# Kernel tuning notes

Measured on AMD Instinct MI355X. Metric: run time of the kernel, lower is better.

Reference implementation:

```python
import jax, jax.numpy as jnp
import numpy as np

RNN = 400
K_WIN = 10      # num_window_mixtures
N_MIX = 20      # num_mixtures
ALPHA = 80      # alphabet_size
IN2 = RNN + ALPHA + 3  # lstm2/lstm3 input size = 483
MDN_OUT = 1 + 6 * N_MIX  # 121


def setup_inputs() -> dict:
    key = jax.random.key(0)
    ks = jax.random.split(key, 20)
    std = 0.075
    B, T, U = 256, 800, 100
    inp = {
        "trajectory": jax.random.normal(ks[0], (B, T, 3), jnp.float32),
        "char_sequence": jax.random.uniform(ks[1], (B, U, ALPHA), jnp.float32),
        # LSTM1 (input 3)
        "w_ih1": jax.random.normal(ks[2], (4 * RNN, 3), jnp.float32) * std,
        "w_hh1": jax.random.normal(ks[3], (4 * RNN, RNN), jnp.float32) * std,
        "b1": jax.random.normal(ks[4], (4 * RNN,), jnp.float32) * std,
        # LSTM2 (input 483)
        "w_ih2": jax.random.normal(ks[5], (4 * RNN, IN2), jnp.float32) * std,
        "w_hh2": jax.random.normal(ks[6], (4 * RNN, RNN), jnp.float32) * std,
        "b2": jax.random.normal(ks[7], (4 * RNN,), jnp.float32) * std,
        # LSTM3 (input 483)
        "w_ih3": jax.random.normal(ks[8], (4 * RNN, IN2), jnp.float32) * std,
        "w_hh3": jax.random.normal(ks[9], (4 * RNN, RNN), jnp.float32) * std,
        "b3": jax.random.normal(ks[10], (4 * RNN,), jnp.float32) * std,
        # window linear (Graves attention), bias init mean -3.0 std 0.25
        "w_win": jax.random.normal(ks[11], (3 * K_WIN, RNN), jnp.float32) * std,
        "b_win": jax.random.normal(ks[12], (3 * K_WIN,), jnp.float32) * 0.25 - 3.0,
        # MDN head
        "w_mdn": jax.random.normal(ks[13], (MDN_OUT, RNN), jnp.float32) * std,
        "b_mdn": jax.random.normal(ks[14], (MDN_OUT,), jnp.float32) * std,
    }
    return inp


def _lstm_cell(x, h, c, w_ih, w_hh, b):
    # torch.nn.LSTMCell gate order: i, f, g, o
    gates = x @ w_ih.T + h @ w_hh.T + b
    i, f, g, o = jnp.split(gates, 4, axis=-1)
    c_new = jax.nn.sigmoid(f) * c + jax.nn.sigmoid(i) * jnp.tanh(g)
    h_new = jax.nn.sigmoid(o) * jnp.tanh(c_new)
    return h_new, c_new


def reference(trajectory, char_sequence,
              w_ih1, w_hh1, b1, w_ih2, w_hh2, b2, w_ih3, w_hh3, b3,
              w_win, b_win, w_mdn, b_mdn):
    B, T, _ = trajectory.shape
    U = char_sequence.shape[1]
    u = jnp.arange(U, dtype=trajectory.dtype)  # [U]

    def step(carry, x_t):
        h1, c1, h2, c2, h3, c3, kappa = carry
        h1, c1 = _lstm_cell(x_t, h1, c1, w_ih1, w_hh1, b1)
        # Gaussian-window attention
        wp = jnp.exp(h1 @ w_win.T + b_win).reshape(B, 3, K_WIN)
        alpha, beta, dkappa = wp[:, 0], wp[:, 1], wp[:, 2]
        kappa = kappa + dkappa
        # phi: [B, U] = sum_k alpha_k * exp(-beta_k * (kappa_k - u)^2)
        diff = kappa[:, :, None] - u[None, None, :]          # [B, K, U]
        phi = jnp.sum(alpha[:, :, None] * jnp.exp(-beta[:, :, None] * diff * diff), axis=1)
        window = jnp.einsum('bu,bua->ba', phi, char_sequence)  # [B, ALPHA]
        x2 = jnp.concatenate([h1, window, x_t], axis=1)
        h2, c2 = _lstm_cell(x2, h2, c2, w_ih2, w_hh2, b2)
        x3 = jnp.concatenate([h2, window, x_t], axis=1)
        h3, c3 = _lstm_cell(x3, h3, c3, w_ih3, w_hh3, b3)
        out = h3 @ w_mdn.T + b_mdn  # [B, 121]
        return (h1, c1, h2, c2, h3, c3, kappa), out

    z = jnp.zeros((B, RNN), trajectory.dtype)
    kappa0 = jnp.zeros((B, K_WIN), trajectory.dtype)
    carry0 = (z, z, z, z, z, z, kappa0)
    _, outs = jax.lax.scan(step, carry0, jnp.swapaxes(trajectory, 0, 1))  # [T, B, 121]
    return jnp.swapaxes(outs, 0, 1)  # [B, T, 121]
```

## Files before the change

### kernel.cpp

```cpp
#include <hip/hip_runtime.h>
#include <hip/hip_bf16.h>

#define RNNU 400
#define NBATCH 256
#define TT 800
#define UU 100
#define ALW 80
#define KW 10
#define K1 416
#define K2 896
#define NBLK 256
#define NTHR 256

typedef unsigned short u16;
typedef unsigned int u32;
typedef __attribute__((ext_vector_type(8))) short bfrag;
typedef __attribute__((ext_vector_type(4))) float f4;

constexpr long P1 = (long)NBATCH * K1;
constexpr long P2 = (long)NBATCH * K2;
constexpr long WP1 = 1600L * K1;
constexpr long WP2 = 1600L * K2;
constexpr long WPM = 128L * K1;
constexpr long WPW = 32L * K1;

constexpr size_t OFF_FLAGS = 0;
constexpr size_t OFF_U1 = 16384;
constexpr size_t OFF_U2 = OFF_U1 + (size_t)4 * P1 * 2;
constexpr size_t OFF_U3 = OFF_U2 + (size_t)4 * P2 * 2;
constexpr size_t OFF_W1 = OFF_U3 + (size_t)4 * P2 * 2;
constexpr size_t OFF_W2 = OFF_W1 + (size_t)2 * WP1 * 2;
constexpr size_t OFF_W3 = OFF_W2 + (size_t)2 * WP2 * 2;
constexpr size_t OFF_WM = OFF_W3 + (size_t)2 * WP2 * 2;
constexpr size_t OFF_WW = OFF_WM + (size_t)2 * WPM * 2;
constexpr size_t OFF_PB1 = OFF_WW + (size_t)2 * WPW * 2;
constexpr size_t OFF_PB2 = OFF_PB1 + 6400;
constexpr size_t OFF_PB3 = OFF_PB2 + 6400;
constexpr size_t OFF_C1 = OFF_PB3 + 6400;
constexpr size_t OFF_C2 = OFF_C1 + 409600;
constexpr size_t OFF_C3 = OFF_C2 + 409600;
constexpr size_t OFF_KP = OFF_C3 + 409600;

__device__ __forceinline__ u16 f2b(float x) {
  union { float f; u32 u; } v; v.f = x;
  u32 r = (v.u + 0x7FFFu + ((v.u >> 16) & 1u)) >> 16;
  return (u16)r;
}
__device__ __forceinline__ float b2f(u16 h) {
  union { u32 u; float f; } q; q.u = ((u32)h) << 16; return q.f;
}
__device__ __forceinline__ void wsp2(u16* base, long plane, long idx, float v) {
  u16 hi = f2b(v);
  base[idx] = hi;
  base[plane + idx] = f2b(v - b2f(hi));
}
__device__ __forceinline__ float sigf(float x) { return 1.f / (1.f + __expf(-x)); }
__device__ __forceinline__ float tanhf_(float x) {
  float e = __expf(-2.f * x); return (1.f - e) / (1.f + e);
}

__global__ void prep_kernel(
    const float* __restrict__ w_ih1, const float* __restrict__ w_hh1, const float* __restrict__ b1,
    const float* __restrict__ w_ih2, const float* __restrict__ w_hh2, const float* __restrict__ b2,
    const float* __restrict__ w_ih3, const float* __restrict__ w_hh3, const float* __restrict__ b3,
    const float* __restrict__ w_win, const float* __restrict__ w_mdn,
    const float* __restrict__ traj, char* __restrict__ ws)
{
  u16* W1 = (u16*)(ws + OFF_W1);
  u16* W2 = (u16*)(ws + OFF_W2);
  u16* W3 = (u16*)(ws + OFF_W3);
  u16* WM = (u16*)(ws + OFF_WM);
  u16* WW = (u16*)(ws + OFF_WW);

  const long N1 = WP1, N2 = WP2, N3 = WP2;
  const long N4 = WPM, N5 = WPW, N6 = 4800, N7 = 307200, N8 = 2560, N9 = 4096;
  const long N10 = P1, N11 = (long)NBATCH * RNNU, N12 = (long)NBATCH * RNNU;
  const long total = N1 + N2 + N3 + N4 + N5 + N6 + N7 + N8 + N9 + N10 + N11 + N12;

  for (long i = (long)blockIdx.x * blockDim.x + threadIdx.x; i < total;
       i += (long)gridDim.x * blockDim.x) {
    long j = i;
    if (j < N1) { int n = (int)(j / K1), k = (int)(j % K1);
      int s = (n & 3) * 400 + (n >> 2);
      float v = (k < 3) ? w_ih1[s * 3 + k] : ((k >= 16) ? w_hh1[(long)s * 400 + (k - 16)] : 0.f);
      wsp2(W1, WP1, j, v); continue; } j -= N1;
    if (j < N2) { int n = (int)(j / K2), k = (int)(j % K2);
      int s = (n & 3) * 400 + (n >> 2);
      float v = (k < 483) ? w_ih2[(long)s * 483 + k] : ((k >= 496) ? w_hh2[(long)s * 400 + (k - 496)] : 0.f);
      wsp2(W2, WP2, j, v); continue; } j -= N2;
    if (j < N3) { int n = (int)(j / K2), k = (int)(j % K2);
      int s = (n & 3) * 400 + (n >> 2);
      float v = (k < 483) ? w_ih3[(long)s * 483 + k] : ((k >= 496) ? w_hh3[(long)s * 400 + (k - 496)] : 0.f);
      wsp2(W3, WP2, j, v); continue; } j -= N3;
    if (j < N4) { int n = (int)(j / K1), k = (int)(j % K1);
      float v = (n < 121 && k >= 16) ? w_mdn[(long)n * 400 + (k - 16)] : 0.f;
      wsp2(WM, WPM, j, v); continue; } j -= N4;
    if (j < N5) { int n = (int)(j / K1), k = (int)(j % K1);
      float v = (n < 30 && k < 400) ? w_win[(long)n * 400 + k] : 0.f;
      wsp2(WW, WPW, j, v); continue; } j -= N5;
    if (j < N6) { int w = (int)(j / 1600), n = (int)(j % 1600);
      int s = (n & 3) * 400 + (n >> 2);
      float* pb = (float*)(ws + (w == 0 ? OFF_PB1 : (w == 1 ? OFF_PB2 : OFF_PB3)));
      const float* bb = (w == 0 ? b1 : (w == 1 ? b2 : b3));
      pb[n] = bb[s]; continue; } j -= N6;
    if (j < N7) { ((float*)(ws + OFF_C1))[j] = 0.f; continue; } j -= N7;
    if (j < N8) { ((float*)(ws + OFF_KP))[j] = 0.f; continue; } j -= N8;
    if (j < N9) { ((u32*)(ws + OFF_FLAGS))[j] = 0u; continue; } j -= N9;
    if (j < N10) { int r = (int)(j / K1), k = (int)(j % K1);
      u16* U1 = (u16*)(ws + OFF_U1);
      float v = (k < 3) ? traj[(long)r * 2400 + k] : 0.f;
      wsp2(U1, P1, j, v); continue; } j -= N10;
    if (j < N11) { int r = (int)(j / 400), k = (int)(j % 400);
      u16* U2 = (u16*)(ws + OFF_U2);
      long idx = (long)r * K2 + 496 + k;
      U2[idx] = 0; U2[P2 + idx] = 0; continue; } j -= N11;
    { int r = (int)(j / 400), k = (int)(j % 400);
      u16* U3 = (u16*)(ws + OFF_U3);
      long idx = (long)r * K2 + 496 + k;
      U3[idx] = 0; U3[P2 + idx] = 0; }
  }
}

__device__ __forceinline__ void gridbar(u32* flags, u32 e, int bid, int tid) {
  __syncthreads();
  if (tid == 0) {
    __threadfence();
    __hip_atomic_store(&flags[bid * 16], e, __ATOMIC_RELEASE, __HIP_MEMORY_SCOPE_AGENT);
  }
  u32* f = &flags[tid * 16];
  while (__hip_atomic_load(f, __ATOMIC_RELAXED, __HIP_MEMORY_SCOPE_AGENT) < e) {
    __builtin_amdgcn_s_sleep(1);
  }
  __threadfence();
  __syncthreads();
}

template<int NK, int KPAD>
__device__ __forceinline__ void gemm_gate_tile(
    int rt, int ct, const u16* __restrict__ Abase, long APS,
    const u16* __restrict__ Wbase, long WPS,
    const float* __restrict__ pbias, float* __restrict__ cst,
    u16* __restrict__ hd0, int st0, long ps0,
    u16* __restrict__ hd1, int st1, long ps1,
    float* __restrict__ ldsb, int lane)
{
  const int r0 = rt * 32, c0 = ct * 80;
  f4 acc[2][5];
#pragma unroll
  for (int a = 0; a < 2; a++)
#pragma unroll
    for (int b = 0; b < 5; b++) acc[a][b] = (f4)(0.f);

  const long aoff = (long)(r0 + (lane & 15)) * KPAD + ((lane >> 4) * 8);
  const long woff = (long)(c0 + (lane & 15)) * KPAD + ((lane >> 4) * 8);

#pragma unroll 1
  for (int pass = 0; pass < 3; ++pass) {
    const u16* Ap0 = Abase + ((pass == 2) ? APS : 0) + aoff;
    const u16* Ap1 = Ap0 + 16 * KPAD;
    const u16* Wp  = Wbase + ((pass == 1) ? WPS : 0) + woff;
#pragma unroll
    for (int kb = 0; kb < NK; ++kb) {
      bfrag a0 = *(const bfrag*)(Ap0 + kb * 32);
      bfrag a1 = *(const bfrag*)(Ap1 + kb * 32);
#pragma unroll
      for (int cf = 0; cf < 5; ++cf) {
        bfrag bf = *(const bfrag*)(Wp + (long)cf * 16 * KPAD + kb * 32);
        acc[0][cf] = __builtin_amdgcn_mfma_f32_16x16x32_bf16(a0, bf, acc[0][cf], 0, 0, 0);
        acc[1][cf] = __builtin_amdgcn_mfma_f32_16x16x32_bf16(a1, bf, acc[1][cf], 0, 0, 0);
      }
    }
  }
  const int cl = lane & 15, rq = lane >> 4;
#pragma unroll
  for (int rf = 0; rf < 2; ++rf)
#pragma unroll
    for (int cf = 0; cf < 5; ++cf) {
      float bias = pbias[c0 + cf * 16 + cl];
#pragma unroll
      for (int r = 0; r < 4; ++r)
        ldsb[(rf * 16 + rq * 4 + r) * 80 + cf * 16 + cl] = acc[rf][cf][r] + bias;
    }
  asm volatile("s_waitcnt lgkmcnt(0)" ::: "memory");
#pragma unroll
  for (int q = 0; q < 10; ++q) {
    int idx = q * 64 + lane;
    int rl = idx / 20, ul = idx % 20;
    float gi = ldsb[rl * 80 + 4 * ul + 0];
    float gf = ldsb[rl * 80 + 4 * ul + 1];
    float gg = ldsb[rl * 80 + 4 * ul + 2];
    float go = ldsb[rl * 80 + 4 * ul + 3];
    long row = r0 + rl; int unit = ct * 20 + ul;
    long ci = row * 400 + unit;
    float cn = sigf(gf) * cst[ci] + sigf(gi) * tanhf_(gg);
    cst[ci] = cn;
    float hv = sigf(go) * tanhf_(cn);
    u16 hh = f2b(hv);
    u16 hl = f2b(hv - b2f(hh));
    long i0 = row * st0 + unit;
    hd0[i0] = hh; hd0[ps0 + i0] = hl;
    if (hd1) { long i1 = row * st1 + unit; hd1[i1] = hh; hd1[ps1 + i1] = hl; }
  }
}

__device__ __forceinline__ void mdn_tile(
    int mt, const u16* __restrict__ Abase, long APS,
    const u16* __restrict__ Wm, long WPS,
    const float* __restrict__ b_mdn, float* __restrict__ out, int tcol, int lane)
{
  const int r0 = mt * 16;
  f4 acc[8];
#pragma unroll
  for (int c = 0; c < 8; c++) acc[c] = (f4)(0.f);
  const long aoff = (long)(r0 + (lane & 15)) * K2 + ((lane >> 4) * 8);
  const long woff = (long)(lane & 15) * K1 + ((lane >> 4) * 8);
#pragma unroll 1
  for (int pass = 0; pass < 3; ++pass) {
    const u16* Ap = Abase + ((pass == 2) ? APS : 0) + aoff;
    const u16* Wp = Wm + ((pass == 1) ? WPS : 0) + woff;
#pragma unroll
    for (int kb = 0; kb < 13; ++kb) {
      bfrag a = *(const bfrag*)(Ap + kb * 32);
#pragma unroll
      for (int cf = 0; cf < 8; ++cf) {
        bfrag b = *(const bfrag*)(Wp + (long)cf * 16 * K1 + kb * 32);
        acc[cf] = __builtin_amdgcn_mfma_f32_16x16x32_bf16(a, b, acc[cf], 0, 0, 0);
      }
    }
  }
  const int cl = lane & 15, rq = lane >> 4;
#pragma unroll
  for (int cf = 0; cf < 8; ++cf) {
    int col = cf * 16 + cl;
    if (col < 121) {
      float bias = b_mdn[col];
#pragma unroll
      for (int r = 0; r < 4; ++r) {
        long row = r0 + rq * 4 + r;
        out[(row * TT + tcol) * 121 + col] = acc[cf][r] + bias;
      }
    }
  }
}

__global__ void __launch_bounds__(NTHR) handw_kernel(
    const float* __restrict__ traj, const float* __restrict__ chars,
    const float* __restrict__ b_win, const float* __restrict__ b_mdn,
    float* __restrict__ out, char* __restrict__ ws)
{
  u32* flags = (u32*)(ws + OFF_FLAGS);
  u16* U1b = (u16*)(ws + OFF_U1);
  u16* U2b = (u16*)(ws + OFF_U2);
  u16* U3b = (u16*)(ws + OFF_U3);
  const u16* W1 = (const u16*)(ws + OFF_W1);
  const u16* W2 = (const u16*)(ws + OFF_W2);
  const u16* W3 = (const u16*)(ws + OFF_W3);
  const u16* WM = (const u16*)(ws + OFF_WM);
  const u16* WW = (const u16*)(ws + OFF_WW);
  const float* PB1 = (const float*)(ws + OFF_PB1);
  const float* PB2 = (const float*)(ws + OFF_PB2);
  const float* PB3 = (const float*)(ws + OFF_PB3);
  float* C1 = (float*)(ws + OFF_C1);
  float* C2 = (float*)(ws + OFF_C2);
  float* C3 = (float*)(ws + OFF_C3);
  float* KP = (float*)(ws + OFF_KP);

  __shared__ float ldseb[2][32 * 80];
  __shared__ float ldswp[16 * 32];
  __shared__ float ldsal[16 * KW];
  __shared__ float ldsbe[16 * KW];
  __shared__ float ldskp[16 * KW];
  __shared__ float ldsphi[16 * UU];

  const int bid = blockIdx.x, tid = threadIdx.x;
  const int wid = tid >> 6, lane = tid & 63;
  u32 epoch = 0;
  const int gtile = (wid < 2 && bid < 80) ? (wid * 80 + bid) : -1;
  const int rt = (gtile >= 0) ? gtile / 20 : 0;
  const int ct = (gtile >= 0) ? gtile % 20 : 0;

  for (int t = 0; t < TT; ++t) {
    const int p = t & 1;
    u16* U1p = U1b + (size_t)p * 2 * P1;
    u16* U1n = U1b + (size_t)(p ^ 1) * 2 * P1;
    u16* U2p = U2b + (size_t)p * 2 * P2;
    u16* U2n = U2b + (size_t)(p ^ 1) * 2 * P2;
    u16* U3p = U3b + (size_t)p * 2 * P2;
    u16* U3n = U3b + (size_t)(p ^ 1) * 2 * P2;

    if (gtile >= 0)
      gemm_gate_tile<13, K1>(rt, ct, U1p, P1, W1, WP1, PB1, C1,
                             U1n + 16, K1, P1, U2p, K2, P2, ldseb[wid], lane);
    if (t > 0 && wid == 0 && bid >= 80 && bid < 96)
      mdn_tile(bid - 80, U3p + 480, P2, WM, WPM, b_mdn, out, t - 1, lane);
    gridbar(flags, ++epoch, bid, tid);

    if (bid < 16) {
      const int r0 = bid * 16;
      if (wid == 0) {
        f4 wacc[2]; wacc[0] = (f4)(0.f); wacc[1] = (f4)(0.f);
        const long aoff = (long)(r0 + (lane & 15)) * K2 + ((lane >> 4) * 8);
        const long woff = (long)(lane & 15) * K1 + ((lane >> 4) * 8);
#pragma unroll 1
        for (int pass = 0; pass < 3; ++pass) {
          const u16* Ap = U2p + ((pass == 2) ? P2 : 0) + aoff;
          const u16* Wp = WW + ((pass == 1) ? WPW : 0) + woff;
#pragma unroll
          for (int kb = 0; kb < 13; ++kb) {
            bfrag a = *(const bfrag*)(Ap + kb * 32);
            bfrag b0 = *(const bfrag*)(Wp + kb * 32);
            bfrag b1 = *(const bfrag*)(Wp + 16 * K1 + kb * 32);
            wacc[0] = __builtin_amdgcn_mfma_f32_16x16x32_bf16(a, b0, wacc[0], 0, 0, 0);
            wacc[1] = __builtin_amdgcn_mfma_f32_16x16x32_bf16(a, b1, wacc[1], 0, 0, 0);
          }
        }
        const int cl = lane & 15, rq = lane >> 4;
#pragma unroll
        for (int cf = 0; cf < 2; ++cf) {
          int col = cf * 16 + cl;
          float bias = (col < 30) ? b_win[col] : 0.f;
#pragma unroll
          for (int r = 0; r < 4; ++r)
            ldswp[(rq * 4 + r) * 32 + col] = wacc[cf][r] + bias;
        }
      }
      __syncthreads();
      if (tid < 160) {
        int r = tid / 10, k = tid % 10; int row = r0 + r;
        float kap = KP[row * 10 + k] + __expf(ldswp[r * 32 + 20 + k]);
        KP[row * 10 + k] = kap;
        ldskp[r * 10 + k] = kap;
        ldsal[r * 10 + k] = __expf(ldswp[r * 32 + k]);
        ldsbe[r * 10 + k] = __expf(ldswp[r * 32 + 10 + k]);
      } else if (tid < 208) {
        int q = tid - 160; int r = q / 3, c = q % 3; int row = r0 + r;
        float xv = traj[((long)row * TT + t) * 3 + c];
        wsp2(U2p, P2, (long)row * K2 + 480 + c, xv);
        wsp2(U3p, P2, (long)row * K2 + 480 + c, xv);
        if (t + 1 < TT)
          wsp2(U1n, P1, (long)row * K1 + c, traj[((long)row * TT + t + 1) * 3 + c]);
      }
      __syncthreads();
      {
        int r = tid & 15, uq = tid >> 4;
        for (int u = uq; u < UU; u += 16) {
          float s = 0.f;
#pragma unroll
          for (int k = 0; k < KW; ++k) {
            float d = ldskp[r * 10 + k] - (float)u;
            s += ldsal[r * 10 + k] * __expf(-ldsbe[r * 10 + k] * d * d);
          }
          ldsphi[r * UU + u] = s;
        }
      }
      __syncthreads();
      {
        int r = tid >> 4, d0 = tid & 15; int row = r0 + r;
        float w[5] = {0.f, 0.f, 0.f, 0.f, 0.f};
        const float* cb = chars + (long)row * UU * ALW;
        for (int u = 0; u < UU; ++u) {
          float ph = ldsphi[r * UU + u];
#pragma unroll
          for (int jj = 0; jj < 5; ++jj) w[jj] += ph * cb[u * ALW + d0 + 16 * jj];
        }
#pragma unroll
        for (int jj = 0; jj < 5; ++jj) {
          int d = d0 + 16 * jj;
          wsp2(U2p, P2, (long)row * K2 + 400 + d, w[jj]);
          wsp2(U3p, P2, (long)row * K2 + 400 + d, w[jj]);
        }
      }
    }
    gridbar(flags, ++epoch, bid, tid);

    if (gtile >= 0)
      gemm_gate_tile<28, K2>(rt, ct, U2p, P2, W2, WP2, PB2, C2,
                             U3p, K2, P2, U2n + 496, K2, P2, ldseb[wid], lane);
    gridbar(flags, ++epoch, bid, tid);

    if (gtile >= 0)
      gemm_gate_tile<28, K2>(rt, ct, U3p, P2, W3, WP2, PB3, C3,
                             U3n + 496, K2, P2, (u16*)nullptr, 0, 0, ldseb[wid], lane);
    gridbar(flags, ++epoch, bid, tid);
  }
  if (wid == 0 && bid >= 80 && bid < 96)
    mdn_tile(bid - 80, U3b + 480, P2, WM, WPM, b_mdn, out, TT - 1, lane);
}

extern "C" void kernel_launch(void* const* d_in, const int* in_sizes, int n_in,
                              void* d_out, int out_size, void* d_ws, size_t ws_size,
                              hipStream_t stream) {
  const float* traj   = (const float*)d_in[0];
  const float* chars  = (const float*)d_in[1];
  const float* w_ih1  = (const float*)d_in[2];
  const float* w_hh1  = (const float*)d_in[3];
  const float* b1     = (const float*)d_in[4];
  const float* w_ih2  = (const float*)d_in[5];
  const float* w_hh2  = (const float*)d_in[6];
  const float* b2     = (const float*)d_in[7];
  const float* w_ih3  = (const float*)d_in[8];
  const float* w_hh3  = (const float*)d_in[9];
  const float* b3     = (const float*)d_in[10];
  const float* w_win  = (const float*)d_in[11];
  const float* b_win  = (const float*)d_in[12];
  const float* w_mdn  = (const float*)d_in[13];
  const float* b_mdn  = (const float*)d_in[14];
  float* outp = (float*)d_out;
  char* wsp = (char*)d_ws;

  prep_kernel<<<dim3(8192), dim3(256), 0, stream>>>(
      w_ih1, w_hh1, b1, w_ih2, w_hh2, b2, w_ih3, w_hh3, b3, w_win, w_mdn, traj, wsp);

  void* kargs[] = { (void*)&traj, (void*)&chars, (void*)&b_win, (void*)&b_mdn,
                    (void*)&outp, (void*)&wsp };
  hipError_t err = hipLaunchCooperativeKernel((void*)handw_kernel, dim3(NBLK), dim3(NTHR),
                                              kargs, 0, stream);
  if (err != hipSuccess) {
    handw_kernel<<<dim3(NBLK), dim3(NTHR), 0, stream>>>(traj, chars, b_win, b_mdn, outp, wsp);
  }
}
```

Before: 292.9 ms.

## Replace fenced grid barrier with coherent atomics, fuse split-bf16 passes, bf16 char cache

```diff
diff --git a/kernel.cpp b/kernel.cpp
--- a/kernel.cpp
+++ b/kernel.cpp
@@ -14,6 +14,7 @@
 
 typedef unsigned short u16;
 typedef unsigned int u32;
+typedef unsigned long long u64;
 typedef __attribute__((ext_vector_type(8))) short bfrag;
 typedef __attribute__((ext_vector_type(4))) float f4;
 
@@ -23,6 +24,7 @@
 constexpr long WP2 = 1600L * K2;
 constexpr long WPM = 128L * K1;
 constexpr long WPW = 32L * K1;
+constexpr long NCB = (long)NBATCH * UU * ALW;
 
 constexpr size_t OFF_FLAGS = 0;
 constexpr size_t OFF_U1 = 16384;
@@ -40,6 +42,7 @@
 constexpr size_t OFF_C2 = OFF_C1 + 409600;
 constexpr size_t OFF_C3 = OFF_C2 + 409600;
 constexpr size_t OFF_KP = OFF_C3 + 409600;
+constexpr size_t OFF_CB = OFF_KP + 16384;
 
 __device__ __forceinline__ u16 f2b(float x) {
   union { float f; u32 u; } v; v.f = x;
@@ -53,6 +56,19 @@
   u16 hi = f2b(v);
   base[idx] = hi;
   base[plane + idx] = f2b(v - b2f(hi));
+}
+__device__ __forceinline__ void wsp2c(u16* base, long plane, long idx, float v) {
+  u16 hi = f2b(v);
+  __hip_atomic_store(base + idx, hi, __ATOMIC_RELAXED, __HIP_MEMORY_SCOPE_AGENT);
+  __hip_atomic_store(base + plane + idx, f2b(v - b2f(hi)), __ATOMIC_RELAXED, __HIP_MEMORY_SCOPE_AGENT);
+}
+__device__ __forceinline__ void st_coh16(u16* p, u16 v) {
+  __hip_atomic_store(p, v, __ATOMIC_RELAXED, __HIP_MEMORY_SCOPE_AGENT);
+}
+__device__ __forceinline__ bfrag ld_frag_coh(const u16* p) {
+  u64 lo = __hip_atomic_load((const u64*)p, __ATOMIC_RELAXED, __HIP_MEMORY_SCOPE_AGENT);
+  u64 hi = __hip_atomic_load((const u64*)(p + 4), __ATOMIC_RELAXED, __HIP_MEMORY_SCOPE_AGENT);
+  union { u64 q[2]; bfrag f; } u; u.q[0] = lo; u.q[1] = hi; return u.f;
 }
 __device__ __forceinline__ float sigf(float x) { return 1.f / (1.f + __expf(-x)); }
 __device__ __forceinline__ float tanhf_(float x) {
@@ -64,18 +80,19 @@
     const float* __restrict__ w_ih2, const float* __restrict__ w_hh2, const float* __restrict__ b2,
     const float* __restrict__ w_ih3, const float* __restrict__ w_hh3, const float* __restrict__ b3,
     const float* __restrict__ w_win, const float* __restrict__ w_mdn,
-    const float* __restrict__ traj, char* __restrict__ ws)
+    const float* __restrict__ traj, const float* __restrict__ chars, char* __restrict__ ws)
 {
   u16* W1 = (u16*)(ws + OFF_W1);
   u16* W2 = (u16*)(ws + OFF_W2);
   u16* W3 = (u16*)(ws + OFF_W3);
   u16* WM = (u16*)(ws + OFF_WM);
   u16* WW = (u16*)(ws + OFF_WW);
+  u16* CB = (u16*)(ws + OFF_CB);
 
   const long N1 = WP1, N2 = WP2, N3 = WP2;
   const long N4 = WPM, N5 = WPW, N6 = 4800, N7 = 307200, N8 = 2560, N9 = 4096;
-  const long N10 = P1, N11 = (long)NBATCH * RNNU, N12 = (long)NBATCH * RNNU;
-  const long total = N1 + N2 + N3 + N4 + N5 + N6 + N7 + N8 + N9 + N10 + N11 + N12;
+  const long N10 = P1, N11 = (long)NBATCH * RNNU, N12 = (long)NBATCH * RNNU, N13 = NCB;
+  const long total = N1 + N2 + N3 + N4 + N5 + N6 + N7 + N8 + N9 + N10 + N11 + N12 + N13;
 
   for (long i = (long)blockIdx.x * blockDim.x + threadIdx.x; i < total;
        i += (long)gridDim.x * blockDim.x) {
@@ -114,24 +131,22 @@
       u16* U2 = (u16*)(ws + OFF_U2);
       long idx = (long)r * K2 + 496 + k;
       U2[idx] = 0; U2[P2 + idx] = 0; continue; } j -= N11;
-    { int r = (int)(j / 400), k = (int)(j % 400);
+    if (j < N12) { int r = (int)(j / 400), k = (int)(j % 400);
       u16* U3 = (u16*)(ws + OFF_U3);
       long idx = (long)r * K2 + 496 + k;
-      U3[idx] = 0; U3[P2 + idx] = 0; }
+      U3[idx] = 0; U3[P2 + idx] = 0; continue; } j -= N12;
+    CB[j] = f2b(chars[j]);
   }
 }
 
 __device__ __forceinline__ void gridbar(u32* flags, u32 e, int bid, int tid) {
+  asm volatile("s_waitcnt vmcnt(0)" ::: "memory");
   __syncthreads();
-  if (tid == 0) {
-    __threadfence();
-    __hip_atomic_store(&flags[bid * 16], e, __ATOMIC_RELEASE, __HIP_MEMORY_SCOPE_AGENT);
-  }
+  if (tid == 0)
+    __hip_atomic_store(&flags[bid * 16], e, __ATOMIC_RELAXED, __HIP_MEMORY_SCOPE_AGENT);
   u32* f = &flags[tid * 16];
-  while (__hip_atomic_load(f, __ATOMIC_RELAXED, __HIP_MEMORY_SCOPE_AGENT) < e) {
-    __builtin_amdgcn_s_sleep(1);
-  }
-  __threadfence();
+  while (__hip_atomic_load(f, __ATOMIC_RELAXED, __HIP_MEMORY_SCOPE_AGENT) < e)
+    __builtin_amdgcn_s_sleep(2);
   __syncthreads();
 }
 
@@ -153,22 +168,36 @@
 
   const long aoff = (long)(r0 + (lane & 15)) * KPAD + ((lane >> 4) * 8);
   const long woff = (long)(c0 + (lane & 15)) * KPAD + ((lane >> 4) * 8);
-
-#pragma unroll 1
-  for (int pass = 0; pass < 3; ++pass) {
-    const u16* Ap0 = Abase + ((pass == 2) ? APS : 0) + aoff;
-    const u16* Ap1 = Ap0 + 16 * KPAD;
-    const u16* Wp  = Wbase + ((pass == 1) ? WPS : 0) + woff;
-#pragma unroll
-    for (int kb = 0; kb < NK; ++kb) {
-      bfrag a0 = *(const bfrag*)(Ap0 + kb * 32);
-      bfrag a1 = *(const bfrag*)(Ap1 + kb * 32);
-#pragma unroll
-      for (int cf = 0; cf < 5; ++cf) {
-        bfrag bf = *(const bfrag*)(Wp + (long)cf * 16 * KPAD + kb * 32);
-        acc[0][cf] = __builtin_amdgcn_mfma_f32_16x16x32_bf16(a0, bf, acc[0][cf], 0, 0, 0);
-        acc[1][cf] = __builtin_amdgcn_mfma_f32_16x16x32_bf16(a1, bf, acc[1][cf], 0, 0, 0);
-      }
+  const u16* Ah0 = Abase + aoff;
+  const u16* Ah1 = Ah0 + 16 * KPAD;
+  const u16* Al0 = Abase + APS + aoff;
+  const u16* Al1 = Al0 + 16 * KPAD;
+  const u16* Wh = Wbase + woff;
+  const u16* Wl = Wbase + WPS + woff;
+
+#pragma unroll
+  for (int kb = 0; kb < NK; ++kb) {
+    bfrag a0 = ld_frag_coh(Ah0 + kb * 32);
+    bfrag a1 = ld_frag_coh(Ah1 + kb * 32);
+#pragma unroll
+    for (int cf = 0; cf < 5; ++cf) {
+      bfrag wh = *(const bfrag*)(Wh + (long)cf * 16 * KPAD + kb * 32);
+      bfrag wl = *(const bfrag*)(Wl + (long)cf * 16 * KPAD + kb * 32);
+      acc[0][cf] = __builtin_amdgcn_mfma_f32_16x16x32_bf16(a0, wh, acc[0][cf], 0, 0, 0);
+      acc[1][cf] = __builtin_amdgcn_mfma_f32_16x16x32_bf16(a1, wh, acc[1][cf], 0, 0, 0);
+      acc[0][cf] = __builtin_amdgcn_mfma_f32_16x16x32_bf16(a0, wl, acc[0][cf], 0, 0, 0);
+      acc[1][cf] = __builtin_amdgcn_mfma_f32_16x16x32_bf16(a1, wl, acc[1][cf], 0, 0, 0);
+    }
+  }
+#pragma unroll
+  for (int kb = 0; kb < NK; ++kb) {
+    bfrag a0 = ld_frag_coh(Al0 + kb * 32);
+    bfrag a1 = ld_frag_coh(Al1 + kb * 32);
+#pragma unroll
+    for (int cf = 0; cf < 5; ++cf) {
+      bfrag wh = *(const bfrag*)(Wh + (long)cf * 16 * KPAD + kb * 32);
+      acc[0][cf] = __builtin_amdgcn_mfma_f32_16x16x32_bf16(a0, wh, acc[0][cf], 0, 0, 0);
+      acc[1][cf] = __builtin_amdgcn_mfma_f32_16x16x32_bf16(a1, wh, acc[1][cf], 0, 0, 0);
     }
   }
   const int cl = lane & 15, rq = lane >> 4;
@@ -198,8 +227,8 @@
     u16 hh = f2b(hv);
     u16 hl = f2b(hv - b2f(hh));
     long i0 = row * st0 + unit;
-    hd0[i0] = hh; hd0[ps0 + i0] = hl;
-    if (hd1) { long i1 = row * st1 + unit; hd1[i1] = hh; hd1[ps1 + i1] = hl; }
+    st_coh16(hd0 + i0, hh); st_coh16(hd0 + ps0 + i0, hl);
+    if (hd1) { long i1 = row * st1 + unit; st_coh16(hd1 + i1, hh); st_coh16(hd1 + ps1 + i1, hl); }
   }
 }
 
@@ -214,18 +243,28 @@
   for (int c = 0; c < 8; c++) acc[c] = (f4)(0.f);
   const long aoff = (long)(r0 + (lane & 15)) * K2 + ((lane >> 4) * 8);
   const long woff = (long)(lane & 15) * K1 + ((lane >> 4) * 8);
-#pragma unroll 1
-  for (int pass = 0; pass < 3; ++pass) {
-    const u16* Ap = Abase + ((pass == 2) ? APS : 0) + aoff;
-    const u16* Wp = Wm + ((pass == 1) ? WPS : 0) + woff;
-#pragma unroll
-    for (int kb = 0; kb < 13; ++kb) {
-      bfrag a = *(const bfrag*)(Ap + kb * 32);
-#pragma unroll
-      for (int cf = 0; cf < 8; ++cf) {
-        bfrag b = *(const bfrag*)(Wp + (long)cf * 16 * K1 + kb * 32);
-        acc[cf] = __builtin_amdgcn_mfma_f32_16x16x32_bf16(a, b, acc[cf], 0, 0, 0);
-      }
+  const u16* Ah = Abase + aoff;
+  const u16* Al = Abase + APS + aoff;
+  const u16* Wh = Wm + woff;
+  const u16* Wl = Wm + WPS + woff;
+#pragma unroll
+  for (int kb = 0; kb < 13; ++kb) {
+    bfrag a = ld_frag_coh(Ah + kb * 32);
+#pragma unroll
+    for (int cf = 0; cf < 8; ++cf) {
+      bfrag wh = *(const bfrag*)(Wh + (long)cf * 16 * K1 + kb * 32);
+      bfrag wl = *(const bfrag*)(Wl + (long)cf * 16 * K1 + kb * 32);
+      acc[cf] = __builtin_amdgcn_mfma_f32_16x16x32_bf16(a, wh, acc[cf], 0, 0, 0);
+      acc[cf] = __builtin_amdgcn_mfma_f32_16x16x32_bf16(a, wl, acc[cf], 0, 0, 0);
+    }
+  }
+#pragma unroll
+  for (int kb = 0; kb < 13; ++kb) {
+    bfrag a = ld_frag_coh(Al + kb * 32);
+#pragma unroll
+    for (int cf = 0; cf < 8; ++cf) {
+      bfrag wh = *(const bfrag*)(Wh + (long)cf * 16 * K1 + kb * 32);
+      acc[cf] = __builtin_amdgcn_mfma_f32_16x16x32_bf16(a, wh, acc[cf], 0, 0, 0);
     }
   }
   const int cl = lane & 15, rq = lane >> 4;
@@ -257,6 +296,7 @@
   const u16* W3 = (const u16*)(ws + OFF_W3);
   const u16* WM = (const u16*)(ws + OFF_WM);
   const u16* WW = (const u16*)(ws + OFF_WW);
+  const u16* CB = (const u16*)(ws + OFF_CB);
   const float* PB1 = (const float*)(ws + OFF_PB1);
   const float* PB2 = (const float*)(ws + OFF_PB2);
   const float* PB3 = (const float*)(ws + OFF_PB3);
@@ -301,18 +341,29 @@
         f4 wacc[2]; wacc[0] = (f4)(0.f); wacc[1] = (f4)(0.f);
         const long aoff = (long)(r0 + (lane & 15)) * K2 + ((lane >> 4) * 8);
         const long woff = (long)(lane & 15) * K1 + ((lane >> 4) * 8);
-#pragma unroll 1
-        for (int pass = 0; pass < 3; ++pass) {
-          const u16* Ap = U2p + ((pass == 2) ? P2 : 0) + aoff;
-          const u16* Wp = WW + ((pass == 1) ? WPW : 0) + woff;
-#pragma unroll
-          for (int kb = 0; kb < 13; ++kb) {
-            bfrag a = *(const bfrag*)(Ap + kb * 32);
-            bfrag b0 = *(const bfrag*)(Wp + kb * 32);
-            bfrag b1 = *(const bfrag*)(Wp + 16 * K1 + kb * 32);
-            wacc[0] = __builtin_amdgcn_mfma_f32_16x16x32_bf16(a, b0, wacc[0], 0, 0, 0);
-            wacc[1] = __builtin_amdgcn_mfma_f32_16x16x32_bf16(a, b1, wacc[1], 0, 0, 0);
-          }
+        const u16* Ah = U2p + aoff;
+        const u16* Al = U2p + P2 + aoff;
+        const u16* Wh = WW + woff;
+        const u16* Wl = WW + WPW + woff;
+#pragma unroll
+        for (int kb = 0; kb < 13; ++kb) {
+          bfrag a = ld_frag_coh(Ah + kb * 32);
+          bfrag b0h = *(const bfrag*)(Wh + kb * 32);
+          bfrag b0l = *(const bfrag*)(Wl + kb * 32);
+          bfrag b1h = *(const bfrag*)(Wh + 16 * K1 + kb * 32);
+          bfrag b1l = *(const bfrag*)(Wl + 16 * K1 + kb * 32);
+          wacc[0] = __builtin_amdgcn_mfma_f32_16x16x32_bf16(a, b0h, wacc[0], 0, 0, 0);
+          wacc[0] = __builtin_amdgcn_mfma_f32_16x16x32_bf16(a, b0l, wacc[0], 0, 0, 0);
+          wacc[1] = __builtin_amdgcn_mfma_f32_16x16x32_bf16(a, b1h, wacc[1], 0, 0, 0);
+          wacc[1] = __builtin_amdgcn_mfma_f32_16x16x32_bf16(a, b1l, wacc[1], 0, 0, 0);
+        }
+#pragma unroll
+        for (int kb = 0; kb < 13; ++kb) {
+          bfrag a = ld_frag_coh(Al + kb * 32);
+          bfrag b0h = *(const bfrag*)(Wh + kb * 32);
+          bfrag b1h = *(const bfrag*)(Wh + 16 * K1 + kb * 32);
+          wacc[0] = __builtin_amdgcn_mfma_f32_16x16x32_bf16(a, b0h, wacc[0], 0, 0, 0);
+          wacc[1] = __builtin_amdgcn_mfma_f32_16x16x32_bf16(a, b1h, wacc[1], 0, 0, 0);
         }
         const int cl = lane & 15, rq = lane >> 4;
 #pragma unroll
@@ -335,10 +386,10 @@
       } else if (tid < 208) {
         int q = tid - 160; int r = q / 3, c = q % 3; int row = r0 + r;
         float xv = traj[((long)row * TT + t) * 3 + c];
-        wsp2(U2p, P2, (long)row * K2 + 480 + c, xv);
-        wsp2(U3p, P2, (long)row * K2 + 480 + c, xv);
+        wsp2c(U2p, P2, (long)row * K2 + 480 + c, xv);
+        wsp2c(U3p, P2, (long)row * K2 + 480 + c, xv);
         if (t + 1 < TT)
-          wsp2(U1n, P1, (long)row * K1 + c, traj[((long)row * TT + t + 1) * 3 + c]);
+          wsp2c(U1n, P1, (long)row * K1 + c, traj[((long)row * TT + t + 1) * 3 + c]);
       }
       __syncthreads();
       {
@@ -357,17 +408,18 @@
       {
         int r = tid >> 4, d0 = tid & 15; int row = r0 + r;
         float w[5] = {0.f, 0.f, 0.f, 0.f, 0.f};
-        const float* cb = chars + (long)row * UU * ALW;
+        const u16* cb = CB + (long)row * UU * ALW;
+#pragma unroll 4
         for (int u = 0; u < UU; ++u) {
           float ph = ldsphi[r * UU + u];
 #pragma unroll
-          for (int jj = 0; jj < 5; ++jj) w[jj] += ph * cb[u * ALW + d0 + 16 * jj];
+          for (int jj = 0; jj < 5; ++jj) w[jj] += ph * b2f(cb[u * ALW + d0 + 16 * jj]);
         }
 #pragma unroll
         for (int jj = 0; jj < 5; ++jj) {
           int d = d0 + 16 * jj;
-          wsp2(U2p, P2, (long)row * K2 + 400 + d, w[jj]);
-          wsp2(U3p, P2, (long)row * K2 + 400 + d, w[jj]);
+          wsp2c(U2p, P2, (long)row * K2 + 400 + d, w[jj]);
+          wsp2c(U3p, P2, (long)row * K2 + 400 + d, w[jj]);
         }
       }
     }
@@ -409,7 +461,7 @@
   char* wsp = (char*)d_ws;
 
   prep_kernel<<<dim3(8192), dim3(256), 0, stream>>>(
-      w_ih1, w_hh1, b1, w_ih2, w_hh2, b2, w_ih3, w_hh3, b3, w_win, w_mdn, traj, wsp);
+      w_ih1, w_hh1, b1, w_ih2, w_hh2, b2, w_ih3, w_hh3, b3, w_win, w_mdn, traj, chars, wsp);
 
   void* kargs[] = { (void*)&traj, (void*)&chars, (void*)&b_win, (void*)&b_mdn,
                     (void*)&outp, (void*)&wsp };
```

Result: slower. 321.6 ms (+9.8%).
